# Performance work log

Hardware: AMD Instinct MI355X
Metric: run time of the kernel (lower is better)

The kernel has to match this reference:

```python
import jax, jax.numpy as jnp
import numpy as np

B, D, G, L = 8, 128, 2048, 24
GF = G // 2 + 1  # rfft bins
EPS = 1e-5


def setup_inputs() -> dict:
    key = jax.random.key(0)
    ks = jax.random.split(key, 6)
    x = jax.random.normal(ks[0], (B, D, G), dtype=jnp.float32)
    Phi_f = jax.random.normal(ks[1], (L, GF), dtype=jnp.float32) * 0.1
    Theta = jax.random.normal(ks[2], (L, D, D), dtype=jnp.float32) * (1.0 / np.sqrt(D))
    ln_gamma = jnp.ones((D,), dtype=jnp.float32)
    ln_beta = jnp.zeros((D,), dtype=jnp.float32)
    fc1_w = jax.random.normal(ks[3], (2 * D, D), dtype=jnp.float32) * (1.0 / np.sqrt(D))
    fc1_b = jnp.zeros((2 * D,), dtype=jnp.float32)
    fc2_w = jax.random.normal(ks[4], (D, 2 * D), dtype=jnp.float32) * (1.0 / np.sqrt(2 * D))
    fc2_b = jnp.zeros((D,), dtype=jnp.float32)
    return {
        'x': x, 'Phi_f': Phi_f, 'Theta': Theta,
        'ln_gamma': ln_gamma, 'ln_beta': ln_beta,
        'fc1_w': fc1_w, 'fc1_b': fc1_b, 'fc2_w': fc2_w, 'fc2_b': fc2_b,
    }


def reference(x, Phi_f, Theta, ln_gamma, ln_beta, fc1_w, fc1_b, fc2_w, fc2_b):
    # x: (B, D, G). LayerNorm over the lifting (channel) dim D.
    mean = jnp.mean(x, axis=1, keepdims=True)
    var = jnp.var(x, axis=1, keepdims=True)
    z = (x - mean) * jax.lax.rsqrt(var + EPS)
    z = z * ln_gamma[None, :, None] + ln_beta[None, :, None]

    # Spectral convolution with each Hilbert filter.
    Xf = jnp.fft.rfft(z, axis=-1)                       # (B, D, GF) complex
    Uf = Xf[:, :, None, :] * jnp.conj(Phi_f)[None, None]  # (B, D, L, GF)
    U = jnp.fft.irfft(Uf, n=G, axis=-1)                 # (B, D, L, G)

    # Per-filter channel mixing then reduction over filters:
    # einsum('bdln,lhd->bhln') followed by sum over l, fused:
    S = jnp.einsum('bdlg,lhd->bhg', U, Theta)           # (B, D, G)

    # Pointwise MLP (Conv1d kernel_size=1 == channel matmul).
    H = jnp.einsum('hd,bdg->bhg', fc1_w, S) + fc1_b[None, :, None]
    H = jax.nn.gelu(H, approximate=False)
    out = jnp.einsum('dh,bhg->bdg', fc2_w, H) + fc2_b[None, :, None]
    return x + out
```

## Files before the change

### kernel.cpp

```cpp
#include <hip/hip_runtime.h>
#include <math.h>


#define B_   8
#define D_   128
#define G_   2048
#define L_   24
#define GF_  1025
#define BD_  1024
#define C2_  2050
#define MW_  2176
#define KP2_ 2112
#define DD_  16384

#define PA_CV0 64
#define PA_TT0 130
#define PA_WF0 386
#define PA_WI0 2562
#define PA_END 4610

#define G1_NB  544
#define G1_END 4768

typedef __attribute__((ext_vector_type(8))) short  short8v;
typedef __attribute__((ext_vector_type(4))) float  float4v;

union FU { float f; unsigned int u; };
union V8 { short8v v; ushort u[8]; };
union V4 { uint2 p; ushort u[4]; };

static __device__ __forceinline__ float bf2f(ushort h) {
    FU v; v.u = ((unsigned int)h) << 16; return v.f;
}
static __device__ __forceinline__ ushort f2bf(float f) {
    FU v; v.f = f;
    unsigned int r = v.u + 0x7fffu + ((v.u >> 16) & 1u);
    return (ushort)(r >> 16);
}
static __device__ __forceinline__ void async16(const void* g, void* l) {
    __builtin_amdgcn_global_load_lds(
        (const __attribute__((address_space(1))) void*)g,
        (__attribute__((address_space(3))) void*)l, 16, 0, 0);
}
static __device__ __forceinline__ int is_f32(const unsigned int* graw) {
    return graw[0] == 0x3F800000u;
}

__global__ __launch_bounds__(256) void k_pre(
        const void* __restrict__ x_raw,  const void* __restrict__ th_raw,
        const unsigned int* __restrict__ graw, const void* __restrict__ be_raw,
        const void* __restrict__ w1_raw, const void* __restrict__ b1_raw,
        const void* __restrict__ w2_raw, const void* __restrict__ b2_raw,
        ushort* __restrict__ z,  ushort* __restrict__ wf,
        ushort* __restrict__ wi, ushort* __restrict__ thT,
        ushort* __restrict__ w1c, ushort* __restrict__ b1c,
        ushort* __restrict__ w2c, ushort* __restrict__ b2c) {
    __shared__ ushort T[L_][72];
    int bid = blockIdx.x, tid = threadIdx.x;

    if (bid < PA_CV0) {
        int fl = is_f32(graw);
        int b  = bid >> 3;
        int g  = (bid & 7) * 256 + tid;
        float s = 0.f, ss = 0.f;
        if (fl) {
            const float* xp = (const float*)x_raw + (size_t)b * D_ * G_ + g;
            for (int d = 0; d < D_; ++d) {
                float v = xp[(size_t)d * G_];
                s += v; ss += v * v;
            }
        } else {
            const ushort* xp = (const ushort*)x_raw + (size_t)b * D_ * G_ + g;
            for (int d = 0; d < D_; ++d) {
                float v = bf2f(xp[(size_t)d * G_]);
                s += v; ss += v * v;
            }
        }
        float mean = s * (1.f / D_);
        float var  = ss * (1.f / D_) - mean * mean;
        float inv  = rsqrtf(var + 1e-5f);
        ushort* zp = z + (size_t)b * D_ * G_ + g;
        if (fl) {
            const float* xp = (const float*)x_raw + (size_t)b * D_ * G_ + g;
            const float* gp = (const float*)graw;
            const float* bp = (const float*)be_raw;
            for (int d = 0; d < D_; ++d) {
                float o = (xp[(size_t)d * G_] - mean) * inv * gp[d] + bp[d];
                zp[(size_t)d * G_] = f2bf(o);
            }
        } else {
            const ushort* xp = (const ushort*)x_raw + (size_t)b * D_ * G_ + g;
            const ushort* gp = (const ushort*)graw;
            const ushort* bp = (const ushort*)be_raw;
            for (int d = 0; d < D_; ++d) {
                float o = (bf2f(xp[(size_t)d * G_]) - mean) * inv * bf2f(gp[d])
                        + bf2f(bp[d]);
                zp[(size_t)d * G_] = f2bf(o);
            }
        }
    } else if (bid < PA_TT0) {
        int fl = is_f32(graw);
        int lb = bid - PA_CV0;
        const void* src; ushort* dst; int n, rel;
        if (lb < 32)       { src = w1_raw; dst = w1c; n = 32768; rel = lb; }
        else if (lb == 32) { src = b1_raw; dst = b1c; n = 256;   rel = 0; }
        else if (lb < 65)  { src = w2_raw; dst = w2c; n = 32768; rel = lb - 33; }
        else               { src = b2_raw; dst = b2c; n = 128;   rel = 0; }
        int i0 = rel * 1024 + tid * 4;
        if (fl) {
            const float* s = (const float*)src;
            #pragma unroll
            for (int j = 0; j < 4; ++j) {
                int k = i0 + j;
                if (k < n) dst[k] = f2bf(s[k]);
            }
        } else {
            const ushort* s = (const ushort*)src;
            #pragma unroll
            for (int j = 0; j < 4; ++j) {
                int k = i0 + j;
                if (k < n) dst[k] = s[k];
            }
        }
    } else if (bid < PA_WF0) {
        int fl = is_f32(graw);
        int hd0 = (bid - PA_TT0) * 64;
        if (tid < 192) {
            int l = tid >> 3, c8 = tid & 7;
            V8 o;
            if (fl) {
                const float* tp = (const float*)th_raw + (size_t)l * DD_ +
                                  hd0 + c8 * 8;
                float4v a0 = *(const float4v*)tp;
                float4v a1 = *(const float4v*)(tp + 4);
                #pragma unroll
                for (int j = 0; j < 4; ++j) {
                    o.u[j] = f2bf(a0[j]); o.u[4 + j] = f2bf(a1[j]);
                }
            } else {
                o.v = *(const short8v*)((const ushort*)th_raw +
                                        (size_t)l * DD_ + hd0 + c8 * 8);
            }
            *(short8v*)&T[l][c8 * 8] = o.v;
        }
        __syncthreads();
        int hdl = tid & 63, part = tid >> 6;
        V8 o;
        #pragma unroll
        for (int j = 0; j < 8; ++j) {
            int l = part * 8 + j;
            o.u[j] = (l < L_) ? T[l][hdl] : (ushort)0;
        }
        *(short8v*)(thT + (size_t)(hd0 + hdl) * 32 + part * 8) = o.v;
    } else if (bid < PA_WI0) {
        int c  = bid - PA_WF0;
        int g0 = tid * 8;
        V8 v;
        if (c >= C2_) {
            #pragma unroll
            for (int j = 0; j < 8; ++j) v.u[j] = 0;
        } else {
            int f = c >> 1, im = c & 1;
            #pragma unroll
            for (int j = 0; j < 8; ++j) {
                int g = g0 + j;
                int r = (f * g) & (G_ - 1);
                float th = (float)r * (6.283185307179586f / (float)G_);
                v.u[j] = f2bf(im ? -__sinf(th) : __cosf(th));
            }
        }
        *(short8v*)(wf + (size_t)c * G_ + g0) = v.v;
    } else {
        int g = bid - PA_WI0;
        for (int ch = tid; ch < KP2_ / 8; ch += 256) {
            int c0 = ch * 8;
            V8 v;
            #pragma unroll
            for (int j = 0; j < 8; ++j) {
                int c = c0 + j;
                if (c >= C2_) { v.u[j] = 0; continue; }
                int f = c >> 1, im = c & 1;
                float a = (f == 0 || f == G_ / 2) ? (1.f / G_) : (2.f / G_);
                int r = (f * g) & (G_ - 1);
                float th = (float)r * (6.283185307179586f / (float)G_);
                v.u[j] = f2bf(im ? -a * __sinf(th) : a * __cosf(th));
            }
            *(short8v*)(wi + (size_t)g * KP2_ + c0) = v.v;
        }
    }
}

__global__ __launch_bounds__(256, 4) void k_g1(
        const ushort* __restrict__ wf, const ushort* __restrict__ z,
        float* __restrict__ zft,
        const void* __restrict__ phi_raw, const unsigned int* __restrict__ graw,
        const ushort* __restrict__ thT, ushort* __restrict__ M) {
    __shared__ ushort As[2][64 * 64];
    __shared__ ushort Bs[2][64 * 64];
    __shared__ ushort Aph[16][40];
    int bid = blockIdx.x, tid = threadIdx.x;
    int w = tid >> 6, lane = tid & 63;
    int lr = lane & 15, q = lane >> 4;

    if (bid < G1_NB) {
        int m0 = (bid >> 4) * 64;
        int n0 = (bid & 15) * 64;
        int wm = (w & 1) * 32, wn = (w >> 1) * 32;
        int rl = lane >> 3, c8 = (lane & 7) ^ rl;
        int t0 = w * 2, t1 = w * 2 + 1;
        const ushort* gA0 = wf + (size_t)(m0 + t0 * 8 + rl) * G_ + c8 * 8;
        const ushort* gA1 = wf + (size_t)(m0 + t1 * 8 + rl) * G_ + c8 * 8;
        const ushort* gB0 = z  + (size_t)(n0 + t0 * 8 + rl) * G_ + c8 * 8;
        const ushort* gB1 = z  + (size_t)(n0 + t1 * 8 + rl) * G_ + c8 * 8;

        float4v acc00 = {0.f,0.f,0.f,0.f}, acc01 = {0.f,0.f,0.f,0.f};
        float4v acc10 = {0.f,0.f,0.f,0.f}, acc11 = {0.f,0.f,0.f,0.f};

        async16(gA0, &As[0][t0 * 512]);
        async16(gA1, &As[0][t1 * 512]);
        async16(gB0, &Bs[0][t0 * 512]);
        async16(gB1, &Bs[0][t1 * 512]);
        __syncthreads();

        int buf = 0;
        for (int k0 = 0; k0 < G_; k0 += 64) {
            if (k0 + 64 < G_) {
                int nb = buf ^ 1;
                async16(gA0 + k0 + 64, &As[nb][t0 * 512]);
                async16(gA1 + k0 + 64, &As[nb][t1 * 512]);
                async16(gB0 + k0 + 64, &Bs[nb][t0 * 512]);
                async16(gB1 + k0 + 64, &Bs[nb][t1 * 512]);
            }
            const ushort* Ab = &As[buf][0];
            const ushort* Bb = &Bs[buf][0];
            #pragma unroll
            for (int s = 0; s < 2; ++s) {
                int cs = s * 4 + q;
                int ra0 = wm + lr, ra1 = wm + 16 + lr;
                int rb0 = wn + lr, rb1 = wn + 16 + lr;
                short8v a0 = *(const short8v*)(Ab + ra0 * 64 + ((cs ^ (ra0 & 7)) << 3));
                short8v a1 = *(const short8v*)(Ab + ra1 * 64 + ((cs ^ (ra1 & 7)) << 3));
                short8v b0 = *(const short8v*)(Bb + rb0 * 64 + ((cs ^ (rb0 & 7)) << 3));
                short8v b1 = *(const short8v*)(Bb + rb1 * 64 + ((cs ^ (rb1 & 7)) << 3));
                acc00 = __builtin_amdgcn_mfma_f32_16x16x32_bf16(a0, b0, acc00, 0, 0, 0);
                acc01 = __builtin_amdgcn_mfma_f32_16x16x32_bf16(a0, b1, acc01, 0, 0, 0);
                acc10 = __builtin_amdgcn_mfma_f32_16x16x32_bf16(a1, b0, acc10, 0, 0, 0);
                acc11 = __builtin_amdgcn_mfma_f32_16x16x32_bf16(a1, b1, acc11, 0, 0, 0);
            }
            __syncthreads();
            buf ^= 1;
        }

        float4v accs[2][2] = { { acc00, acc01 }, { acc10, acc11 } };
        #pragma unroll
        for (int i = 0; i < 2; ++i)
            #pragma unroll
            for (int j = 0; j < 2; ++j) {
                int col = n0 + wn + j * 16 + lr;
                int row = m0 + wm + i * 16 + q * 4;
                #pragma unroll
                for (int r = 0; r < 4; ++r)
                    zft[(size_t)(row + r) * BD_ + col] = accs[i][j][r];
            }
    } else {
        int bb  = bid - G1_NB;
        int f0  = (bb >> 6) * 16;
        int hd0 = (bb & 63) * 256;
        int isf = is_f32(graw);
        #pragma unroll
        for (int rep = 0; rep < 2; ++rep) {
            int idx = rep * 256 + tid;
            int fl = idx >> 5, l = idx & 31;
            int f = f0 + fl;
            ushort v = 0;
            if (l < L_ && f < GF_)
                v = isf ? f2bf(((const float*)phi_raw)[(size_t)l * GF_ + f])
                        : ((const ushort*)phi_raw)[(size_t)l * GF_ + f];
            Aph[fl][l] = v;
        }
        __syncthreads();
        short8v a = *(const short8v*)&Aph[lr][q * 8];
        #pragma unroll
        for (int t = 0; t < 4; ++t) {
            int n = hd0 + (w * 4 + t) * 16 + lr;
            short8v b = *(const short8v*)(thT + (size_t)n * 32 + q * 8);
            float4v c = {0.f, 0.f, 0.f, 0.f};
            c = __builtin_amdgcn_mfma_f32_16x16x32_bf16(a, b, c, 0, 0, 0);
            #pragma unroll
            for (int r = 0; r < 4; ++r) {
                int f = f0 + q * 4 + r;
                if (f < GF_) M[(size_t)f * DD_ + n] = f2bf(c[r]);
            }
        }
    }
}

__global__ __launch_bounds__(256, 2) void k_mix3(const float* __restrict__ zft,
                                                 const ushort* __restrict__ M,
                                                 ushort* __restrict__ sft) {
    int f   = blockIdx.x;
    int tid = threadIdx.x;
    int w = tid >> 6, lane = tid & 63;
    int lr = lane & 15, q = lane >> 4;

    int cc = lr >> 3, bb = lr & 7;
    const float* zrow = zft + (size_t)(2 * f + cc) * BD_ + bb * 128 + q * 8;
    short8v a[4];
    #pragma unroll
    for (int s = 0; s < 4; ++s) {
        float4v v0 = *(const float4v*)(zrow + s * 32);
        float4v v1 = *(const float4v*)(zrow + s * 32 + 4);
        V8 t;
        t.u[0] = f2bf(v0[0]); t.u[1] = f2bf(v0[1]);
        t.u[2] = f2bf(v0[2]); t.u[3] = f2bf(v0[3]);
        t.u[4] = f2bf(v1[0]); t.u[5] = f2bf(v1[1]);
        t.u[6] = f2bf(v1[2]); t.u[7] = f2bf(v1[3]);
        a[s] = t.v;
    }

    const ushort* Mf = M + (size_t)f * DD_;
    #pragma unroll
    for (int n = 0; n < 2; ++n) {
        int nt = 2 * w + n;
        float4v c = {0.f, 0.f, 0.f, 0.f};
        #pragma unroll
        for (int s = 0; s < 4; ++s) {
            short8v bfr = *(const short8v*)(Mf + (size_t)(nt * 16 + lr) * D_ +
                                            s * 32 + q * 8);
            c = __builtin_amdgcn_mfma_f32_16x16x32_bf16(a[s], bfr, c, 0, 0, 0);
        }
        #pragma unroll
        for (int r = 0; r < 4; ++r) {
            int p  = q * 4 + r;
            int c2 = p >> 3, b2 = p & 7;
            sft[(size_t)(2 * f + c2) * BD_ + b2 * 128 + nt * 16 + lr] = f2bf(c[r]);
        }
    }
}

__global__ __launch_bounds__(256, 4) void k_gemm64t(const ushort* __restrict__ A,
                                                    const ushort* __restrict__ Bm,
                                                    float* __restrict__ C,
                                                    int K, int lda, int ldb, int ldc) {
    __shared__ ushort As[2][64 * 64];
    __shared__ ushort Bs[2][64 * 64];
    int tid = threadIdx.x;
    int m0 = blockIdx.x * 64, n0 = blockIdx.y * 64;
    int w = tid >> 6, lane = tid & 63;
    int lr = lane & 15, q = lane >> 4;
    int wm = (w & 1) * 32, wn = (w >> 1) * 32;

    int rl = lane >> 3, c8 = (lane & 7) ^ rl;
    int t0 = w * 2, t1 = w * 2 + 1;
    const ushort* gA0 = A + (size_t)(m0 + t0 * 8 + rl) * lda + c8 * 8;
    const ushort* gA1 = A + (size_t)(m0 + t1 * 8 + rl) * lda + c8 * 8;

    int br = tid >> 2;
    int bc = tid & 3;

    float4v acc00 = {0.f,0.f,0.f,0.f}, acc01 = {0.f,0.f,0.f,0.f};
    float4v acc10 = {0.f,0.f,0.f,0.f}, acc11 = {0.f,0.f,0.f,0.f};

    async16(gA0, &As[0][t0 * 512]);
    async16(gA1, &As[0][t1 * 512]);
    {
        V8 u0, u1;
        if (br < C2_) {
            const ushort* gb = Bm + (size_t)br * ldb + n0 + bc * 16;
            u0.v = *(const short8v*)gb;
            u1.v = *(const short8v*)(gb + 8);
        } else {
            #pragma unroll
            for (int j = 0; j < 8; ++j) { u0.u[j] = 0; u1.u[j] = 0; }
        }
        #pragma unroll
        for (int j = 0; j < 8; ++j) {
            int n = bc * 16 + j;
            Bs[0][n * 64 + ((((br >> 3) ^ (n & 7)) << 3) | (br & 7))] = u0.u[j];
        }
        #pragma unroll
        for (int j = 0; j < 8; ++j) {
            int n = bc * 16 + 8 + j;
            Bs[0][n * 64 + ((((br >> 3) ^ (n & 7)) << 3) | (br & 7))] = u1.u[j];
        }
    }
    __syncthreads();

    int buf = 0;
    for (int k0 = 0; k0 < K; k0 += 64) {
        V8 u0, u1;
        bool more = (k0 + 64 < K);
        if (more) {
            int nb = buf ^ 1;
            async16(gA0 + k0 + 64, &As[nb][t0 * 512]);
            async16(gA1 + k0 + 64, &As[nb][t1 * 512]);
            int kr = k0 + 64 + br;
            if (kr < C2_) {
                const ushort* gb = Bm + (size_t)kr * ldb + n0 + bc * 16;
                u0.v = *(const short8v*)gb;
                u1.v = *(const short8v*)(gb + 8);
            } else {
                #pragma unroll
                for (int j = 0; j < 8; ++j) { u0.u[j] = 0; u1.u[j] = 0; }
            }
        }
        const ushort* Ab = &As[buf][0];
        const ushort* Bb = &Bs[buf][0];
        #pragma unroll
        for (int s = 0; s < 2; ++s) {
            int cs = s * 4 + q;
            int ra0 = wm + lr, ra1 = wm + 16 + lr;
            int rb0 = wn + lr, rb1 = wn + 16 + lr;
            short8v a0 = *(const short8v*)(Ab + ra0 * 64 + ((cs ^ (ra0 & 7)) << 3));
            short8v a1 = *(const short8v*)(Ab + ra1 * 64 + ((cs ^ (ra1 & 7)) << 3));
            short8v b0 = *(const short8v*)(Bb + rb0 * 64 + ((cs ^ (rb0 & 7)) << 3));
            short8v b1 = *(const short8v*)(Bb + rb1 * 64 + ((cs ^ (rb1 & 7)) << 3));
            acc00 = __builtin_amdgcn_mfma_f32_16x16x32_bf16(a0, b0, acc00, 0, 0, 0);
            acc01 = __builtin_amdgcn_mfma_f32_16x16x32_bf16(a0, b1, acc01, 0, 0, 0);
            acc10 = __builtin_amdgcn_mfma_f32_16x16x32_bf16(a1, b0, acc10, 0, 0, 0);
            acc11 = __builtin_amdgcn_mfma_f32_16x16x32_bf16(a1, b1, acc11, 0, 0, 0);
        }
        __syncthreads();
        if (more) {
            int nb = buf ^ 1;
            #pragma unroll
            for (int j = 0; j < 8; ++j) {
                int n = bc * 16 + j;
                Bs[nb][n * 64 + ((((br >> 3) ^ (n & 7)) << 3) | (br & 7))] = u0.u[j];
            }
            #pragma unroll
            for (int j = 0; j < 8; ++j) {
                int n = bc * 16 + 8 + j;
                Bs[nb][n * 64 + ((((br >> 3) ^ (n & 7)) << 3) | (br & 7))] = u1.u[j];
            }
        }
        __syncthreads();
        buf ^= 1;
    }

    float4v accs[2][2] = { { acc00, acc01 }, { acc10, acc11 } };
    #pragma unroll
    for (int i = 0; i < 2; ++i)
        #pragma unroll
        for (int j = 0; j < 2; ++j) {
            int col = n0 + wn + j * 16 + lr;
            int row = m0 + wm + i * 16 + q * 4;
            #pragma unroll
            for (int r = 0; r < 4; ++r)
                C[(size_t)(row + r) * ldc + col] = accs[i][j][r];
        }
}

#define MLPG 32
__global__ __launch_bounds__(256, 2) void k_mlp3(const float* __restrict__ ST,
                                                 const void* __restrict__ x0,
                                                 const ushort* __restrict__ w1,
                                                 const ushort* __restrict__ b1,
                                                 const ushort* __restrict__ w2,
                                                 const ushort* __restrict__ b2,
                                                 const unsigned int* __restrict__ graw,
                                                 void* __restrict__ outv) {
    __shared__ ushort Sb[MLPG][136];
    __shared__ ushort Hb[MLPG][264];
    __shared__ float  Ob[128][36];
    int g0 = blockIdx.x * MLPG, b = blockIdx.y;
    int tid = threadIdx.x;
    {
        int col = tid >> 3, seg = tid & 7;
        const float* sp = ST + (size_t)(g0 + col) * BD_ + b * D_ + seg * 16;
        float4v v0 = *(const float4v*)(sp);
        float4v v1 = *(const float4v*)(sp + 4);
        float4v v2 = *(const float4v*)(sp + 8);
        float4v v3 = *(const float4v*)(sp + 12);
        V8 o0, o1;
        #pragma unroll
        for (int k = 0; k < 4; ++k) { o0.u[k] = f2bf(v0[k]); o0.u[4 + k] = f2bf(v1[k]); }
        #pragma unroll
        for (int k = 0; k < 4; ++k) { o1.u[k] = f2bf(v2[k]); o1.u[4 + k] = f2bf(v3[k]); }
        *(short8v*)&Sb[col][seg * 16]     = o0.v;
        *(short8v*)&Sb[col][seg * 16 + 8] = o1.v;
    }
    __syncthreads();
    int w = tid >> 6, lane = tid & 63;
    int lr = lane & 15, q = lane >> 4;
    int nt = w & 1, mh = w >> 1;

    {
        float4v acc[8];
        #pragma unroll
        for (int i = 0; i < 8; ++i) { float4v zz = {0.f,0.f,0.f,0.f}; acc[i] = zz; }
        #pragma unroll
        for (int ks = 0; ks < 4; ++ks) {
            short8v bf = *(const short8v*)&Sb[nt * 16 + lr][ks * 32 + q * 8];
            #pragma unroll
            for (int i = 0; i < 8; ++i) {
                int mt = mh * 8 + i;
                short8v af = *(const short8v*)(w1 + (size_t)(mt * 16 + lr) * D_ +
                                               ks * 32 + q * 8);
                acc[i] = __builtin_amdgcn_mfma_f32_16x16x32_bf16(af, bf, acc[i], 0, 0, 0);
            }
        }
        #pragma unroll
        for (int i = 0; i < 8; ++i) {
            int h0 = (mh * 8 + i) * 16 + q * 4;
            V4 hv;
            #pragma unroll
            for (int r = 0; r < 4; ++r) {
                float v = acc[i][r] + bf2f(b1[h0 + r]);
                v = 0.5f * v * (1.f + erff(v * 0.70710678118f));
                hv.u[r] = f2bf(v);
            }
            *(uint2*)&Hb[nt * 16 + lr][h0] = hv.p;
        }
    }
    __syncthreads();
    {
        float4v acc2[4];
        #pragma unroll
        for (int j = 0; j < 4; ++j) { float4v zz = {0.f,0.f,0.f,0.f}; acc2[j] = zz; }
        #pragma unroll
        for (int ks = 0; ks < 8; ++ks) {
            short8v bf = *(const short8v*)&Hb[nt * 16 + lr][ks * 32 + q * 8];
            #pragma unroll
            for (int j = 0; j < 4; ++j) {
                int mt2 = mh * 4 + j;
                short8v af = *(const short8v*)(w2 + (size_t)(mt2 * 16 + lr) * (2 * D_) +
                                               ks * 32 + q * 8);
                acc2[j] = __builtin_amdgcn_mfma_f32_16x16x32_bf16(af, bf, acc2[j], 0, 0, 0);
            }
        }
        int col = nt * 16 + lr;
        #pragma unroll
        for (int j = 0; j < 4; ++j) {
            int d0 = (mh * 4 + j) * 16 + q * 4;
            #pragma unroll
            for (int r = 0; r < 4; ++r)
                Ob[d0 + r][col] = acc2[j][r] + bf2f(b2[d0 + r]);
        }
    }
    __syncthreads();
    {
        int fl = is_f32(graw);
        if (fl) {
            #pragma unroll
            for (int p = 0; p < 4; ++p) {
                int idx = p * 256 + tid;
                int d = idx >> 3, c4 = (idx & 7) * 4;
                float4v o = *(const float4v*)&Ob[d][c4];
                size_t gidx = ((size_t)(b * D_ + d)) * G_ + g0 + c4;
                float4v xv = *(const float4v*)((const float*)x0 + gidx);
                float4v ov;
                #pragma unroll
                for (int k = 0; k < 4; ++k) ov[k] = o[k] + xv[k];
                *(float4v*)((float*)outv + gidx) = ov;
            }
        } else {
            #pragma unroll
            for (int p = 0; p < 4; ++p) {
                int idx = p * 256 + tid;
                int d = idx >> 3, c4 = (idx & 7) * 4;
                float4v o = *(const float4v*)&Ob[d][c4];
                size_t gidx = ((size_t)(b * D_ + d)) * G_ + g0 + c4;
                V4 xv; xv.p = *(const uint2*)((const ushort*)x0 + gidx);
                V4 ov;
                #pragma unroll
                for (int k = 0; k < 4; ++k) ov.u[k] = f2bf(o[k] + bf2f(xv.u[k]));
                *(uint2*)((ushort*)outv + gidx) = ov.p;
            }
        }
    }
}

extern "C" void kernel_launch(void* const* d_in, const int* in_sizes, int n_in,
                              void* d_out, int out_size, void* d_ws, size_t ws_size,
                              hipStream_t stream) {
    char* base = (char*)d_ws;
    ushort* z    = (ushort*)(base);
    ushort* wf   = (ushort*)(base + 4194304);
    ushort* sft  = (ushort*)(base);
    float*  zft  = (float*)(base + 13107200);
    float*  st   = (float*)(base + 13107200);
    ushort* w1c  = (ushort*)(base + 27050048);
    ushort* b1c  = (ushort*)(base + 27115584);
    ushort* w2c  = (ushort*)(base + 27116096);
    ushort* b2c  = (ushort*)(base + 27181632);
    ushort* Mm   = (ushort*)(base + 27182592);
    ushort* wi   = (ushort*)(base + 60769792);
    ushort* thT  = (ushort*)(base + 69420544);

    const unsigned int* graw = (const unsigned int*)d_in[3];

    k_pre    <<<dim3(PA_END), 256, 0, stream>>>(
        d_in[0], d_in[2], graw, d_in[4], d_in[5], d_in[6], d_in[7], d_in[8],
        z, wf, wi, thT, w1c, b1c, w2c, b2c);
    k_g1     <<<dim3(G1_END), 256, 0, stream>>>(wf, z, zft, d_in[1], graw,
                                                thT, Mm);
    k_mix3   <<<dim3(GF_), 256, 0, stream>>>(zft, Mm, sft);
    k_gemm64t<<<dim3(G_ / 64, BD_ / 64), 256, 0, stream>>>(
        wi, sft, st, KP2_, KP2_, BD_, BD_);
    k_mlp3   <<<dim3(G_ / MLPG, B_), 256, 0, stream>>>(st, d_in[0], w1c, b1c,
                                                       w2c, b2c, graw, d_out);
}
```

Before: 187.6 us.

## Use even/odd split real-FFT trick to halve DFT GEMM sizes

Result: faster. 168.8 us (-10.1%).

```diff
diff --git a/kernel.cpp b/kernel.cpp
--- a/kernel.cpp
+++ b/kernel.cpp
@@ -8,16 +8,17 @@
 #define L_   24
 #define GF_  1025
 #define BD_  1024
-#define C2_  2050
-#define MW_  2176
-#define KP2_ 2112
 #define DD_  16384
+#define GH_  1024
+#define CF_  1026
+#define MF_  1088
+#define NF_  2048
 
 #define PA_CV0 64
 #define PA_TT0 130
 #define PA_WF0 386
-#define PA_WI0 2562
-#define PA_END 4610
+#define PA_WI0 1474
+#define PA_END 2498
 
 #define G1_NB  544
 #define G1_END 4768
@@ -79,14 +80,15 @@
         float mean = s * (1.f / D_);
         float var  = ss * (1.f / D_) - mean * mean;
         float inv  = rsqrtf(var + 1e-5f);
-        ushort* zp = z + (size_t)b * D_ * G_ + g;
+        ushort* zp = z + (size_t)(g & 1) * (BD_ * GH_) +
+                     (size_t)(b * D_) * GH_ + (g >> 1);
         if (fl) {
             const float* xp = (const float*)x_raw + (size_t)b * D_ * G_ + g;
             const float* gp = (const float*)graw;
             const float* bp = (const float*)be_raw;
             for (int d = 0; d < D_; ++d) {
                 float o = (xp[(size_t)d * G_] - mean) * inv * gp[d] + bp[d];
-                zp[(size_t)d * G_] = f2bf(o);
+                zp[(size_t)d * GH_] = f2bf(o);
             }
         } else {
             const ushort* xp = (const ushort*)x_raw + (size_t)b * D_ * G_ + g;
@@ -95,7 +97,7 @@
             for (int d = 0; d < D_; ++d) {
                 float o = (bf2f(xp[(size_t)d * G_]) - mean) * inv * bf2f(gp[d])
                         + bf2f(bp[d]);
-                zp[(size_t)d * G_] = f2bf(o);
+                zp[(size_t)d * GH_] = f2bf(o);
             }
         }
     } else if (bid < PA_TT0) {
@@ -154,38 +156,39 @@
         *(short8v*)(thT + (size_t)(hd0 + hdl) * 32 + part * 8) = o.v;
     } else if (bid < PA_WI0) {
         int c  = bid - PA_WF0;
-        int g0 = tid * 8;
-        V8 v;
-        if (c >= C2_) {
-            #pragma unroll
-            for (int j = 0; j < 8; ++j) v.u[j] = 0;
+        int g0 = tid * 4;
+        V4 v;
+        if (c >= CF_) {
+            #pragma unroll
+            for (int j = 0; j < 4; ++j) v.u[j] = 0;
         } else {
             int f = c >> 1, im = c & 1;
             #pragma unroll
-            for (int j = 0; j < 8; ++j) {
+            for (int j = 0; j < 4; ++j) {
                 int g = g0 + j;
-                int r = (f * g) & (G_ - 1);
-                float th = (float)r * (6.283185307179586f / (float)G_);
+                int r = (f * g) & (GH_ - 1);
+                float th = (float)r * 6.135923151542565e-3f;
                 v.u[j] = f2bf(im ? -__sinf(th) : __cosf(th));
             }
         }
-        *(short8v*)(wf + (size_t)c * G_ + g0) = v.v;
+        *(uint2*)(wf + (size_t)c * GH_ + g0) = v.p;
     } else {
         int g = bid - PA_WI0;
-        for (int ch = tid; ch < KP2_ / 8; ch += 256) {
+        for (int ch = tid; ch < MF_ / 8; ch += 256) {
             int c0 = ch * 8;
             V8 v;
             #pragma unroll
             for (int j = 0; j < 8; ++j) {
                 int c = c0 + j;
-                if (c >= C2_) { v.u[j] = 0; continue; }
+                if (c >= CF_) { v.u[j] = 0; continue; }
                 int f = c >> 1, im = c & 1;
-                float a = (f == 0 || f == G_ / 2) ? (1.f / G_) : (2.f / G_);
-                int r = (f * g) & (G_ - 1);
-                float th = (float)r * (6.283185307179586f / (float)G_);
+                float a = (f == 0 || f == GH_ / 2) ? (1.f / 2048.f)
+                                                   : (1.f / 1024.f);
+                int r = (f * g) & (GH_ - 1);
+                float th = (float)r * 6.135923151542565e-3f;
                 v.u[j] = f2bf(im ? -a * __sinf(th) : a * __cosf(th));
             }
-            *(short8v*)(wi + (size_t)g * KP2_ + c0) = v.v;
+            *(short8v*)(wi + (size_t)g * MF_ + c0) = v.v;
         }
     }
 }
@@ -203,15 +206,15 @@
     int lr = lane & 15, q = lane >> 4;
 
     if (bid < G1_NB) {
-        int m0 = (bid >> 4) * 64;
-        int n0 = (bid & 15) * 64;
+        int m0 = (bid >> 5) * 64;
+        int n0 = (bid & 31) * 64;
         int wm = (w & 1) * 32, wn = (w >> 1) * 32;
         int rl = lane >> 3, c8 = (lane & 7) ^ rl;
         int t0 = w * 2, t1 = w * 2 + 1;
-        const ushort* gA0 = wf + (size_t)(m0 + t0 * 8 + rl) * G_ + c8 * 8;
-        const ushort* gA1 = wf + (size_t)(m0 + t1 * 8 + rl) * G_ + c8 * 8;
-        const ushort* gB0 = z  + (size_t)(n0 + t0 * 8 + rl) * G_ + c8 * 8;
-        const ushort* gB1 = z  + (size_t)(n0 + t1 * 8 + rl) * G_ + c8 * 8;
+        const ushort* gA0 = wf + (size_t)(m0 + t0 * 8 + rl) * GH_ + c8 * 8;
+        const ushort* gA1 = wf + (size_t)(m0 + t1 * 8 + rl) * GH_ + c8 * 8;
+        const ushort* gB0 = z  + (size_t)(n0 + t0 * 8 + rl) * GH_ + c8 * 8;
+        const ushort* gB1 = z  + (size_t)(n0 + t1 * 8 + rl) * GH_ + c8 * 8;
 
         float4v acc00 = {0.f,0.f,0.f,0.f}, acc01 = {0.f,0.f,0.f,0.f};
         float4v acc10 = {0.f,0.f,0.f,0.f}, acc11 = {0.f,0.f,0.f,0.f};
@@ -223,8 +226,8 @@
         __syncthreads();
 
         int buf = 0;
-        for (int k0 = 0; k0 < G_; k0 += 64) {
-            if (k0 + 64 < G_) {
+        for (int k0 = 0; k0 < GH_; k0 += 64) {
+            if (k0 + 64 < GH_) {
                 int nb = buf ^ 1;
                 async16(gA0 + k0 + 64, &As[nb][t0 * 512]);
                 async16(gA1 + k0 + 64, &As[nb][t1 * 512]);
@@ -260,7 +263,7 @@
                 int row = m0 + wm + i * 16 + q * 4;
                 #pragma unroll
                 for (int r = 0; r < 4; ++r)
-                    zft[(size_t)(row + r) * BD_ + col] = accs[i][j][r];
+                    zft[(size_t)(row + r) * NF_ + col] = accs[i][j][r];
             }
     } else {
         int bb  = bid - G1_NB;
@@ -298,42 +301,79 @@
 __global__ __launch_bounds__(256, 2) void k_mix3(const float* __restrict__ zft,
                                                  const ushort* __restrict__ M,
                                                  ushort* __restrict__ sft) {
-    int f   = blockIdx.x;
+    int fp  = blockIdx.x;
+    int fb  = GH_ - fp;
     int tid = threadIdx.x;
     int w = tid >> 6, lane = tid & 63;
     int lr = lane & 15, q = lane >> 4;
-
     int cc = lr >> 3, bb = lr & 7;
-    const float* zrow = zft + (size_t)(2 * f + cc) * BD_ + bb * 128 + q * 8;
-    short8v a[4];
+
+    float ang = (float)fp * 3.0679615757712823e-3f;
+    float wr  = cosf(ang), sn = sinf(ang);
+    float wi_ = -sn;
+    float wsig = cc ? wi_ : -wi_;
+    float cbv  = cc ? wr  : -wr;
+    float asgn = cc ? -1.f : 1.f;
+
+    const float* rc = zft + (size_t)(2 * fp + cc) * NF_;
+    const float* ro = zft + (size_t)(2 * fp + (cc ^ 1)) * NF_;
+    int colb = bb * 128 + q * 8;
+
+    short8v aZ[4], aZb[4];
     #pragma unroll
     for (int s = 0; s < 4; ++s) {
-        float4v v0 = *(const float4v*)(zrow + s * 32);
-        float4v v1 = *(const float4v*)(zrow + s * 32 + 4);
-        V8 t;
-        t.u[0] = f2bf(v0[0]); t.u[1] = f2bf(v0[1]);
-        t.u[2] = f2bf(v0[2]); t.u[3] = f2bf(v0[3]);
-        t.u[4] = f2bf(v1[0]); t.u[5] = f2bf(v1[1]);
-        t.u[6] = f2bf(v1[2]); t.u[7] = f2bf(v1[3]);
-        a[s] = t.v;
-    }
-
-    const ushort* Mf = M + (size_t)f * DD_;
+        int col = colb + s * 32;
+        float4v av0 = *(const float4v*)(rc + col);
+        float4v av1 = *(const float4v*)(rc + col + 4);
+        float4v bv0 = *(const float4v*)(rc + BD_ + col);
+        float4v bv1 = *(const float4v*)(rc + BD_ + col + 4);
+        float4v bo0 = *(const float4v*)(ro + BD_ + col);
+        float4v bo1 = *(const float4v*)(ro + BD_ + col + 4);
+        V8 tz, tb;
+        #pragma unroll
+        for (int j = 0; j < 4; ++j) {
+            float av = av0[j], bv = bv0[j], bo = bo0[j];
+            float zz = fmaf(wsig, bo, fmaf(wr, bv, av));
+            float zb = fmaf(cbv, bv, fmaf(wi_, bo, asgn * av));
+            tz.u[j] = f2bf(zz); tb.u[j] = f2bf(zb);
+            av = av1[j]; bv = bv1[j]; bo = bo1[j];
+            zz = fmaf(wsig, bo, fmaf(wr, bv, av));
+            zb = fmaf(cbv, bv, fmaf(wi_, bo, asgn * av));
+            tz.u[4 + j] = f2bf(zz); tb.u[4 + j] = f2bf(zb);
+        }
+        aZ[s] = tz.v; aZb[s] = tb.v;
+    }
+
+    const ushort* Mf = M + (size_t)fp * DD_;
+    const ushort* Mb = M + (size_t)fb * DD_;
     #pragma unroll
     for (int n = 0; n < 2; ++n) {
         int nt = 2 * w + n;
-        float4v c = {0.f, 0.f, 0.f, 0.f};
+        float4v c1 = {0.f, 0.f, 0.f, 0.f};
+        float4v c2 = {0.f, 0.f, 0.f, 0.f};
         #pragma unroll
         for (int s = 0; s < 4; ++s) {
-            short8v bfr = *(const short8v*)(Mf + (size_t)(nt * 16 + lr) * D_ +
-                                            s * 32 + q * 8);
-            c = __builtin_amdgcn_mfma_f32_16x16x32_bf16(a[s], bfr, c, 0, 0, 0);
+            short8v b1 = *(const short8v*)(Mf + (size_t)(nt * 16 + lr) * D_ +
+                                           s * 32 + q * 8);
+            short8v b2 = *(const short8v*)(Mb + (size_t)(nt * 16 + lr) * D_ +
+                                           s * 32 + q * 8);
+            c1 = __builtin_amdgcn_mfma_f32_16x16x32_bf16(aZ[s],  b1, c1, 0, 0, 0);
+            c2 = __builtin_amdgcn_mfma_f32_16x16x32_bf16(aZb[s], b2, c2, 0, 0, 0);
         }
         #pragma unroll
         for (int r = 0; r < 4; ++r) {
-            int p  = q * 4 + r;
-            int c2 = p >> 3, b2 = p & 7;
-            sft[(size_t)(2 * f + c2) * BD_ + b2 * 128 + nt * 16 + lr] = f2bf(c[r]);
+            int p   = q * 4 + r;
+            int c2i = p >> 3, b2 = p & 7;
+            float sgm = c2i ? -1.f : 1.f;
+            float se  = c1[r] + sgm * c2[r];
+            float sop = c1[r] - sgm * c2[r];
+            float pp  = __shfl_xor(sop, 32);
+            float tsg = c2i ? sn : -sn;
+            float so  = fmaf(tsg, pp, sop * wr);
+            size_t rowo = (size_t)(2 * fp + c2i) * NF_;
+            int colh = b2 * 128 + nt * 16 + lr;
+            sft[rowo + colh]       = f2bf(se);
+            sft[rowo + BD_ + colh] = f2bf(so);
         }
     }
 }
@@ -341,7 +381,8 @@
 __global__ __launch_bounds__(256, 4) void k_gemm64t(const ushort* __restrict__ A,
                                                     const ushort* __restrict__ Bm,
                                                     float* __restrict__ C,
-                                                    int K, int lda, int ldb, int ldc) {
+                                                    int K, int lda, int ldb,
+                                                    int ldc, int kv) {
     __shared__ ushort As[2][64 * 64];
     __shared__ ushort Bs[2][64 * 64];
     int tid = threadIdx.x;
@@ -365,7 +406,7 @@
     async16(gA1, &As[0][t1 * 512]);
     {
         V8 u0, u1;
-        if (br < C2_) {
+        if (br < kv) {
             const ushort* gb = Bm + (size_t)br * ldb + n0 + bc * 16;
             u0.v = *(const short8v*)gb;
             u1.v = *(const short8v*)(gb + 8);
@@ -395,7 +436,7 @@
             async16(gA0 + k0 + 64, &As[nb][t0 * 512]);
             async16(gA1 + k0 + 64, &As[nb][t1 * 512]);
             int kr = k0 + 64 + br;
-            if (kr < C2_) {
+            if (kr < kv) {
                 const ushort* gb = Bm + (size_t)kr * ldb + n0 + bc * 16;
                 u0.v = *(const short8v*)gb;
                 u1.v = *(const short8v*)(gb + 8);
@@ -467,7 +508,9 @@
     int tid = threadIdx.x;
     {
         int col = tid >> 3, seg = tid & 7;
-        const float* sp = ST + (size_t)(g0 + col) * BD_ + b * D_ + seg * 16;
+        int g = g0 + col;
+        const float* sp = ST + (size_t)(g >> 1) * NF_ + (g & 1) * BD_ +
+                          b * D_ + seg * 16;
         float4v v0 = *(const float4v*)(sp);
         float4v v1 = *(const float4v*)(sp + 4);
         float4v v2 = *(const float4v*)(sp + 8);
@@ -595,9 +638,9 @@
         z, wf, wi, thT, w1c, b1c, w2c, b2c);
     k_g1     <<<dim3(G1_END), 256, 0, stream>>>(wf, z, zft, d_in[1], graw,
                                                 thT, Mm);
-    k_mix3   <<<dim3(GF_), 256, 0, stream>>>(zft, Mm, sft);
-    k_gemm64t<<<dim3(G_ / 64, BD_ / 64), 256, 0, stream>>>(
-        wi, sft, st, KP2_, KP2_, BD_, BD_);
+    k_mix3   <<<dim3(513), 256, 0, stream>>>(zft, Mm, sft);
+    k_gemm64t<<<dim3(GH_ / 64, NF_ / 64), 256, 0, stream>>>(
+        wi, sft, st, MF_, MF_, NF_, NF_, CF_);
     k_mlp3   <<<dim3(G_ / MLPG, B_), 256, 0, stream>>>(st, d_in[0], w1c, b1c,
                                                        w2c, b2c, graw, d_out);
 }
```
